# Performance work log

Hardware: AMD Instinct MI355X
Metric: run time of the kernel (lower is better)

## Reference

```python
import jax, jax.numpy as jnp
import numpy as np

B, C, F, T = 4, 64, 128, 128
K = 8        # kernel_size
H = 32       # lstm hidden size
L = 4        # lstm layers
EPS = 1e-5


def setup_inputs() -> dict:
    key = jax.random.key(0)
    ks = jax.random.split(key, 12)
    f = lambda k, s: jax.random.normal(k, s, dtype=jnp.float32) * 0.1
    return dict(
        x=jax.random.normal(ks[0], (B, C, F, T), dtype=jnp.float32),
        gamma=jnp.ones((C,), jnp.float32),
        beta=jnp.zeros((C,), jnp.float32),
        # layer 0 (input size C*K), stacked over 2 directions
        w_ih0=f(ks[1], (2, 4 * H, C * K)),
        w_hh0=f(ks[2], (2, 4 * H, H)),
        b_ih0=f(ks[3], (2, 4 * H)),
        b_hh0=f(ks[4], (2, 4 * H)),
        # layers 1..L-1 (input size 2*H), stacked [L-1, 2dirs, ...]
        w_ih=f(ks[5], (L - 1, 2, 4 * H, 2 * H)),
        w_hh=f(ks[6], (L - 1, 2, 4 * H, H)),
        b_ih=f(ks[7], (L - 1, 2, 4 * H)),
        b_hh=f(ks[8], (L - 1, 2, 4 * H)),
        # ConvTranspose1d weight, torch layout [in=2H, out=C, K]
        wct=f(ks[9], (2 * H, C, K)),
        bct=f(ks[10], (C,)),
    )


def _lstm_dir(gx, whh, reverse):
    # gx: [S, N, 4H] precomputed input projections (+ both biases)
    Hh = whh.shape[1]
    N = gx.shape[1]

    def step(carry, g):
        h, c = carry
        g = g + h @ whh.T
        i, fg, gg, o = jnp.split(g, 4, axis=-1)  # torch gate order i,f,g,o
        c = jax.nn.sigmoid(fg) * c + jax.nn.sigmoid(i) * jnp.tanh(gg)
        h = jax.nn.sigmoid(o) * jnp.tanh(c)
        return (h, c), h

    init = (jnp.zeros((N, Hh), gx.dtype), jnp.zeros((N, Hh), gx.dtype))
    _, hs = jax.lax.scan(step, init, gx, reverse=reverse)
    return hs  # [S, N, H], time-aligned with input


def _bilstm(xs, wih, whh, bih, bhh):
    outs = []
    for d, rev in ((0, False), (1, True)):
        gx = jnp.einsum('sni,gi->sng', xs, wih[d]) + bih[d] + bhh[d]
        outs.append(_lstm_dir(gx, whh[d], rev))
    return jnp.concatenate(outs, axis=-1)  # [S, N, 2H]


def reference(x, gamma, beta, w_ih0, w_hh0, b_ih0, b_hh0,
              w_ih, w_hh, b_ih, b_hh, wct, bct):
    x = jnp.swapaxes(x, -1, -2)  # [B, C, T, F]
    res = x
    Bb, Cc, Tt, Ff = x.shape
    # InstanceNorm2d (affine, biased variance over (T,F))
    mu = jnp.mean(x, axis=(2, 3), keepdims=True)
    var = jnp.var(x, axis=(2, 3), keepdims=True)
    xn = (x - mu) * jax.lax.rsqrt(var + EPS)
    xn = xn * gamma[None, :, None, None] + beta[None, :, None, None]
    # [B,F,C,T] -> [B*F, C, T]
    xf = jnp.transpose(xn, (0, 3, 1, 2)).reshape(Bb * Ff, Cc, Tt)
    # unfold(dim=2, size=K, step=1): [BF, C, T', K]
    Tp = Tt - K + 1
    idx = jnp.arange(Tp)[:, None] + jnp.arange(K)[None, :]
    seq = jnp.transpose(xf[:, :, idx], (2, 0, 1, 3)).reshape(Tp, Bb * Ff, Cc * K)
    # 4-layer bidirectional LSTM
    h = _bilstm(seq, w_ih0, w_hh0, b_ih0, b_hh0)
    for l in range(w_ih.shape[0]):
        h = _bilstm(h, w_ih[l], w_hh[l], b_ih[l], b_hh[l])
    # [S, BF, 2H] -> [BF, 2H, S]
    h = jnp.transpose(h, (1, 2, 0))
    # ConvTranspose1d stride=1, pad=0: out length = S + K - 1 = T
    y = jax.lax.conv_transpose(
        h, wct, strides=(1,), padding='VALID',
        dimension_numbers=('NCH', 'IOH', 'NCH'), transpose_kernel=True)
    y = y + bct[None, :, None]
    y = y.reshape(Bb, Ff, Cc, Tt)
    y = jnp.transpose(y, (0, 2, 3, 1)) + res  # [B, C, T, F]
    return jnp.swapaxes(y, -1, -2)  # back to [B, C, F, T]
```

## Files before the change

kernel.cpp:

```cpp
#include <hip/hip_runtime.h>

#define B_ 4
#define C_ 64
#define F_ 128
#define T_ 128
#define K_ 8
#define H_ 32
#define S_ 121
#define N_ 512
#define G_ 128
#define CK_ 512

typedef __attribute__((ext_vector_type(8))) short short8;
typedef __attribute__((ext_vector_type(4))) float f32x4;
typedef __attribute__((ext_vector_type(2))) float f32x2;
typedef __attribute__((ext_vector_type(2))) unsigned int ui2;
union FragU { uint4 u; short8 s; };

__device__ __forceinline__ unsigned int pk2(float a, float b){
  unsigned int ua = __float_as_uint(a); ua += 0x7fffu + ((ua>>16)&1u);
  unsigned int ub = __float_as_uint(b); ub += 0x7fffu + ((ub>>16)&1u);
  return (ua>>16) | (ub & 0xffff0000u);
}
__device__ __forceinline__ unsigned short bfu(float a){
  unsigned int ua = __float_as_uint(a); ua += 0x7fffu + ((ua>>16)&1u);
  return (unsigned short)(ua>>16);
}

__device__ __forceinline__ int gslot(int g){ return ((g & 63) << 1) | (g >> 6); }

__global__ __launch_bounds__(256) void k_norm(const float* __restrict__ x,
    const float* __restrict__ gamma, const float* __restrict__ beta,
    float* __restrict__ scale, float* __restrict__ shift){
  int bc = blockIdx.x;
  const float* p = x + (size_t)bc * (F_*T_);
  float s = 0.f, q = 0.f;
  for (int i = threadIdx.x; i < F_*T_; i += 256){ float v = p[i]; s += v; q += v*v; }
  #pragma unroll
  for (int o = 32; o; o >>= 1){ s += __shfl_down(s, o); q += __shfl_down(q, o); }
  __shared__ float ss[4], qq[4];
  int w = threadIdx.x >> 6;
  if ((threadIdx.x & 63) == 0){ ss[w] = s; qq[w] = q; }
  __syncthreads();
  if (threadIdx.x == 0){
    s = ss[0]+ss[1]+ss[2]+ss[3]; q = qq[0]+qq[1]+qq[2]+qq[3];
    float mu  = s / (float)(F_*T_);
    float var = q / (float)(F_*T_) - mu*mu;
    if (var < 0.f) var = 0.f;
    int c = bc & (C_-1);
    float sc = gamma[c] * rsqrtf(var + 1e-5f);
    scale[bc] = sc;
    shift[bc] = beta[c] - mu * sc;
  }
}

__global__ __launch_bounds__(256) void k_wcvt(const float* __restrict__ a,
    unsigned short* __restrict__ o, int nel){
  int i = blockIdx.x*256 + threadIdx.x;
  if (i < nel) o[i] = bfu(a[i]);
}
__global__ __launch_bounds__(256) void k_wrev(const float* __restrict__ a,
    unsigned short* __restrict__ o, int nel){
  int i = blockIdx.x*256 + threadIdx.x;
  if (i < nel){ int j = (i & ~7) | (7 - (i & 7)); o[i] = bfu(a[j]); }
}

__global__ __launch_bounds__(256) void k_gx0(const float* __restrict__ x,
    const float* __restrict__ scale, const float* __restrict__ shift,
    const unsigned short* __restrict__ wb0, const float* __restrict__ bi,
    const float* __restrict__ bh, unsigned short* __restrict__ gx){
  __shared__ unsigned int xsp[C_][80];
  int n = blockIdx.x >> 1, half = blockIdx.x & 1;
  int b = n >> 7, f = n & 127;
  const float* xb = x + (size_t)b*C_*F_*T_ + (size_t)f*T_;
  for (int i = threadIdx.x; i < C_*18; i += 256){
    int c = i / 18, q = i - c*18;
    int t0 = half*64 + q*4;
    float sc = scale[b*C_+c], sh = shift[b*C_+c];
    const float* xr = xb + (size_t)c*F_*T_;
    float4 v = (float4){0.f,0.f,0.f,0.f};
    float e = 0.f;
    bool in4 = (t0 < T_);
    if (in4) v = *(const float4*)(xr + t0);
    if (t0 + 4 < T_) e = xr[t0 + 4];
    float u0 = in4 ? v.x*sc+sh : 0.f;
    float u1 = in4 ? v.y*sc+sh : 0.f;
    float u2 = in4 ? v.z*sc+sh : 0.f;
    float u3 = in4 ? v.w*sc+sh : 0.f;
    float u4 = (t0+4 < T_) ? e*sc+sh : 0.f;
    unsigned int* xc = &xsp[c][q*4];
    xc[0] = pk2(u0,u1); xc[1] = pk2(u1,u2); xc[2] = pk2(u2,u3); xc[3] = pk2(u3,u4);
  }
  __syncthreads();
  int lane = threadIdx.x & 63, wv = threadIdx.x >> 6;
  int ln = lane & 15, quad = lane >> 4;
  int g256[4]; f32x4 acc[4][4];
  #pragma unroll
  for (int gi = 0; gi < 4; ++gi){
    g256[gi] = (wv*4 + gi)*16 + ln;
    float bv = bi[g256[gi]] + bh[g256[gi]];
    #pragma unroll
    for (int stl = 0; stl < 4; ++stl) acc[stl][gi] = (f32x4){bv, bv, bv, bv};
  }
  FragU bcur[4], bnxt[4];
  #pragma unroll
  for (int gi = 0; gi < 4; ++gi)
    bcur[gi].u = *(const uint4*)(wb0 + (size_t)g256[gi]*CK_ + quad*8);
  for (int kb = 0; kb < 16; ++kb){
    if (kb < 15){
      #pragma unroll
      for (int gi = 0; gi < 4; ++gi)
        bnxt[gi].u = *(const uint4*)(wb0 + (size_t)g256[gi]*CK_ + (kb+1)*32 + quad*8);
    }
    #pragma unroll
    for (int stl = 0; stl < 4; ++stl){
      FragU a;
      const unsigned int* rp = &xsp[kb*4 + quad][stl*16 + ln];
      a.u.x = rp[0]; a.u.y = rp[2]; a.u.z = rp[4]; a.u.w = rp[6];
      #pragma unroll
      for (int gi = 0; gi < 4; ++gi)
        acc[stl][gi] = __builtin_amdgcn_mfma_f32_16x16x32_bf16(a.s, bcur[gi].s, acc[stl][gi], 0, 0, 0);
    }
    #pragma unroll
    for (int gi = 0; gi < 4; ++gi) bcur[gi] = bnxt[gi];
  }
  #pragma unroll
  for (int stl = 0; stl < 4; ++stl)
    #pragma unroll
    for (int gi = 0; gi < 4; ++gi){
      int d = g256[gi] >> 7, g = g256[gi] & 127;
      #pragma unroll
      for (int r = 0; r < 4; ++r){
        int s = (half*4 + stl)*16 + quad*4 + r;
        if (s < S_)
          gx[((size_t)(d*N_ + n)*S_ + s)*G_ + gslot(g)] = bfu(acc[stl][gi][r]);
      }
    }
}

__global__ __launch_bounds__(128)
__attribute__((amdgpu_waves_per_eu(1, 1)))
void k_mega(const unsigned short* __restrict__ gx,
    const float* __restrict__ whh0,
    const unsigned short* __restrict__ wlb,
    const float* __restrict__ bih, const float* __restrict__ bhh,
    const float* __restrict__ whh,
    unsigned short* __restrict__ hout){
  __shared__ unsigned int rawA[64][68];
  __shared__ unsigned int rawB[64][68];
  __shared__ unsigned int glds[2][32][66];
  __shared__ unsigned int hsp[32][136];

  int n = blockIdx.x;
  int tid = threadIdx.x;
  int lane = tid & 63, d = tid >> 6;
  int j = lane & 31, hi = lane >> 5;
  int ln = lane & 15, quad = lane >> 4;

  f32x2 w1[16], w2[16];
  float hv = 0.f, c = 0.f;
  unsigned int hgd[4];
  auto rl = [&](int k)->float{
    return __uint_as_float(__builtin_amdgcn_readlane(__float_as_uint(hv), k));
  };
  auto step = [&](unsigned int cur, int u){
    float gg1 = __uint_as_float(cur << 16);
    float gg2 = __uint_as_float(cur & 0xffff0000u);
    f32x2 A1 = {gg1, 0.f}, B1 = {0.f, 0.f};
    f32x2 A2 = {gg2, 0.f}, B2 = {0.f, 0.f};
    #pragma unroll
    for (int m = 0; m < 16; m += 2){
      f32x2 h0; h0.x = rl(2*m);   h0.y = rl(2*m+1);
      f32x2 h1; h1.x = rl(2*m+2); h1.y = rl(2*m+3);
      A1 += h0*w1[m];   A2 += h0*w2[m];
      B1 += h1*w1[m+1]; B2 += h1*w2[m+1];
    }
    float acc1 = (A1.x + B1.x) + (A1.y + B1.y);
    float acc2 = (A2.x + B2.x) + (A2.y + B2.y);
    float a1 = 1.f/(1.f + __expf(-acc1));
    float x2 = hi ? acc2 : 2.f*acc2;
    float tt = 1.f/(1.f + __expf(-x2));
    float a2 = hi ? tt : 2.f*tt - 1.f;
    ui2 p1 = __builtin_amdgcn_permlane32_swap(__float_as_uint(a1), __float_as_uint(a1), false, false);
    ui2 p2 = __builtin_amdgcn_permlane32_swap(__float_as_uint(a2), __float_as_uint(a2), false, false);
    float i_ = __uint_as_float(p1.x);
    float f_ = __uint_as_float(p1.y);
    float g_ = __uint_as_float(p2.x);
    float o_ = __uint_as_float(p2.y);
    c = f_*c + i_*g_;
    float tc = 1.f/(1.f + __expf(-2.f*c));
    hv = o_*(2.f*tc - 1.f);
    unsigned int hb = (unsigned int)bfu(hv);
    if ((u & 1) == 0) hgd[u >> 1] = hb;
    else              hgd[u >> 1] |= hb << 16;
  };
  auto loadw = [&](const float* wr1, const float* wr2){
    #pragma unroll
    for (int q = 0; q < 8; ++q){
      float4 aa = *(const float4*)(wr1 + q*4);
      float4 bb = *(const float4*)(wr2 + q*4);
      w1[q*2+0] = (f32x2){aa.x, aa.y}; w1[q*2+1] = (f32x2){aa.z, aa.w};
      w2[q*2+0] = (f32x2){bb.x, bb.y}; w2[q*2+1] = (f32x2){bb.z, bb.w};
    }
    #pragma unroll
    for (int k = 0; k < 16; ++k){
      asm volatile("" : "+v"(w1[k]));
      asm volatile("" : "+v"(w2[k]));
    }
  };

  {
    loadw(whh0 + (size_t)(d*G_ + lane)*H_, whh0 + (size_t)(d*G_ + lane + 64)*H_);
    const unsigned int* gxu = (const unsigned int*)gx;
    ptrdiff_t stride = d ? -64 : 64;
    const unsigned int* p0 = gxu + ((size_t)(d*N_ + n)*S_ + (d ? (S_-1) : 0))*64 + lane;
    unsigned short* hrow = (unsigned short*)&rawA[d*32 + j][0];
    unsigned int bufA[8], bufB[8];
    #pragma unroll
    for (int u = 0; u < 8; ++u) bufA[u] = p0[stride*u];
    for (int gg = 0; gg < 7; ++gg){
      int g0 = gg*2;
      #pragma unroll
      for (int u = 0; u < 8; ++u) bufB[u] = p0[stride*(8*(g0+1) + u)];
      #pragma unroll
      for (int u = 0; u < 8; ++u) step(bufA[u], u);
      if (!hi) *(uint4*)(hrow + 8*g0) = (uint4){hgd[0], hgd[1], hgd[2], hgd[3]};
      #pragma unroll
      for (int u = 0; u < 8; ++u) bufA[u] = p0[stride*(8*(g0+2) + u)];
      #pragma unroll
      for (int u = 0; u < 8; ++u) step(bufB[u], u);
      if (!hi) *(uint4*)(hrow + 8*(g0+1)) = (uint4){hgd[0], hgd[1], hgd[2], hgd[3]};
    }
    bufB[0] = p0[stride*120];
    #pragma unroll
    for (int u = 0; u < 8; ++u) step(bufA[u], u);
    if (!hi) *(uint4*)(hrow + 112) = (uint4){hgd[0], hgd[1], hgd[2], hgd[3]};
    step(bufB[0], 0);
    if (!hi) hrow[120] = (unsigned short)(hgd[0] & 0xffffu);
  }
  __syncthreads();

  unsigned int (*rin)[68]  = rawA;
  unsigned int (*rout)[68] = rawB;
  for (int l = 0; l < 3; ++l){
    const unsigned short* rawu = (const unsigned short*)&rin[0][0];
    for (int i = tid; i < 32*128; i += 128){
      int srow = i >> 5, ip = i & 31;
      unsigned int v = 0;
      if (srow <= 120){
        int st = (ip < 16) ? srow : (120 - srow);
        v = (unsigned int)rawu[(2*ip)*136 + st] | ((unsigned int)rawu[(2*ip+1)*136 + st] << 16);
      }
      hsp[ip][srow] = v;
    }
    __syncthreads();

    const unsigned short* wp = wlb + (size_t)((l*2 + d)*G_)*64;
    float bias[8];
    const float* bip = bih + (size_t)(l*2 + d)*G_;
    const float* bhp = bhh + (size_t)(l*2 + d)*G_;
    #pragma unroll
    for (int gt = 0; gt < 8; ++gt) bias[gt] = bip[gt*16 + ln] + bhp[gt*16 + ln];
    loadw(whh + (size_t)((l*2 + d)*G_ + lane)*H_,
          whh + (size_t)((l*2 + d)*G_ + lane + 64)*H_);

    FragU bfrc[8][2];
    #pragma unroll
    for (int gt = 0; gt < 8; ++gt){
      bfrc[gt][0].u = *(const uint4*)(wp + (size_t)(gt*16 + ln)*64 + quad*8);
      bfrc[gt][1].u = *(const uint4*)(wp + (size_t)(gt*16 + ln)*64 + 32 + quad*8);
    }

    unsigned short* hrow = (unsigned short*)&rout[d*32 + j][0];
    const unsigned int* gr = &glds[d][0][lane];
    hv = 0.f; c = 0.f;

    for (int ch = 0; ch < 4; ++ch){
      int c0 = d ? (89 - 32*ch) : (32*ch);
      FragU af[2][2];
      #pragma unroll
      for (int stl = 0; stl < 2; ++stl){
        int srow = c0 + stl*16 + ln; if (srow < 0) srow = 0;
        #pragma unroll
        for (int kb = 0; kb < 2; ++kb){
          int ipb = kb*16 + quad*4;
          af[stl][kb].u.x = hsp[ipb+0][srow];
          af[stl][kb].u.y = hsp[ipb+1][srow];
          af[stl][kb].u.z = hsp[ipb+2][srow];
          af[stl][kb].u.w = hsp[ipb+3][srow];
        }
      }
      #pragma unroll
      for (int stl = 0; stl < 2; ++stl)
        #pragma unroll
        for (int gt2 = 0; gt2 < 4; ++gt2){
          f32x4 alo = (f32x4){bias[gt2],   bias[gt2],   bias[gt2],   bias[gt2]};
          f32x4 ahi = (f32x4){bias[gt2+4], bias[gt2+4], bias[gt2+4], bias[gt2+4]};
          alo = __builtin_amdgcn_mfma_f32_16x16x32_bf16(af[stl][0].s, bfrc[gt2  ][0].s, alo, 0, 0, 0);
          alo = __builtin_amdgcn_mfma_f32_16x16x32_bf16(af[stl][1].s, bfrc[gt2  ][1].s, alo, 0, 0, 0);
          ahi = __builtin_amdgcn_mfma_f32_16x16x32_bf16(af[stl][0].s, bfrc[gt2+4][0].s, ahi, 0, 0, 0);
          ahi = __builtin_amdgcn_mfma_f32_16x16x32_bf16(af[stl][1].s, bfrc[gt2+4][1].s, ahi, 0, 0, 0);
          #pragma unroll
          for (int r = 0; r < 4; ++r){
            int off = stl*16 + quad*4 + r;
            int ul = d ? (31 - off) : off;
            glds[d][ul][gt2*16 + ln] = pk2(alo[r], ahi[r]);
          }
        }
      asm volatile("" ::: "memory");
      int nfull = (ch < 3) ? 4 : 3;
      for (int gq = 0; gq < nfull; ++gq){
        unsigned int bv[8];
        #pragma unroll
        for (int u = 0; u < 8; ++u) bv[u] = gr[(gq*8 + u)*66];
        #pragma unroll
        for (int u = 0; u < 8; ++u) step(bv[u], u);
        if (!hi) *(uint4*)(hrow + ch*32 + gq*8) = (uint4){hgd[0], hgd[1], hgd[2], hgd[3]};
      }
      if (ch == 3){
        unsigned int bv0 = gr[24*66];
        step(bv0, 0);
        if (!hi) hrow[120] = (unsigned short)(hgd[0] & 0xffffu);
      }
      asm volatile("" ::: "memory");
    }
    __syncthreads();
    unsigned int (*t)[68] = rin; rin = rout; rout = t;
  }

  unsigned int* ho = (unsigned int*)hout + (size_t)n*64*64;
  for (int i = tid; i < 64*64; i += 128){
    int ci = i >> 6, k = i & 63;
    ho[ci*64 + k] = rin[ci][k];
  }
}

__global__ __launch_bounds__(256) void k_conv(const unsigned short* __restrict__ hin,
    const unsigned short* __restrict__ wA, const float* __restrict__ bct,
    const float* __restrict__ x, float* __restrict__ out){
  __shared__ unsigned int hrawL[64][65];
  __shared__ unsigned int hp2[64][144];
  int n = blockIdx.x, b = n >> 7, f = n & 127;
  const unsigned int* hu = (const unsigned int*)hin + (size_t)n*64*64;
  for (int i = threadIdx.x; i < 64*64; i += 256){
    int ci = i >> 6, k = i & 63;
    hrawL[ci][k] = hu[ci*64 + k];
  }
  __syncthreads();
  const unsigned short* rawu = (const unsigned short*)&hrawL[0][0];
  for (int it = threadIdx.x; it < 64*136; it += 256){
    int ci = it / 136, col = it - ci*136;
    int t0 = col - 8;
    int i0 = (ci < 32) ? t0 : (120 - t0);
    int i1 = (ci < 32) ? (t0+1) : (119 - t0);
    unsigned int lo  = (t0   >= 0 && t0   <= 120) ? rawu[ci*130 + i0] : 0u;
    unsigned int hi2 = (t0+1 >= 0 && t0+1 <= 120) ? rawu[ci*130 + i1] : 0u;
    hp2[ci][col] = lo | (hi2 << 16);
  }
  __syncthreads();
  int lane = threadIdx.x & 63, wv = threadIdx.x >> 6;
  int ln = lane & 15, quad = lane >> 4;
  const unsigned short* wp = wA + (size_t)(wv*16 + ln)*512;
  f32x4 acc[8];
  #pragma unroll
  for (int nt = 0; nt < 8; ++nt) acc[nt] = (f32x4){0.f,0.f,0.f,0.f};
  for (int kb = 0; kb < 16; ++kb){
    FragU afr; afr.u = *(const uint4*)(wp + kb*32 + quad*8);
    int ci = kb*4 + quad;
    #pragma unroll
    for (int nt = 0; nt < 8; ++nt){
      FragU bfr;
      const unsigned int* rp = &hp2[ci][nt*16 + ln + 1];
      bfr.u.x = rp[0]; bfr.u.y = rp[2]; bfr.u.z = rp[4]; bfr.u.w = rp[6];
      acc[nt] = __builtin_amdgcn_mfma_f32_16x16x32_bf16(afr.s, bfr.s, acc[nt], 0, 0, 0);
    }
  }
  float bb[4];
  #pragma unroll
  for (int r = 0; r < 4; ++r) bb[r] = bct[wv*16 + quad*4 + r];
  #pragma unroll
  for (int nt = 0; nt < 8; ++nt)
    #pragma unroll
    for (int r = 0; r < 4; ++r){
      int co = wv*16 + quad*4 + r, t = nt*16 + ln;
      size_t idx = ((size_t)(b*64 + co)*128 + f)*128 + t;
      out[idx] = acc[nt][r] + bb[r] + x[idx];
    }
}

extern "C" void kernel_launch(void* const* d_in, const int* in_sizes, int n_in,
                              void* d_out, int out_size, void* d_ws, size_t ws_size,
                              hipStream_t stream){
  const float* x     = (const float*)d_in[0];
  const float* gamma = (const float*)d_in[1];
  const float* beta  = (const float*)d_in[2];
  const float* wih0  = (const float*)d_in[3];
  const float* whh0  = (const float*)d_in[4];
  const float* bih0  = (const float*)d_in[5];
  const float* bhh0  = (const float*)d_in[6];
  const float* wih   = (const float*)d_in[7];
  const float* whh   = (const float*)d_in[8];
  const float* bih   = (const float*)d_in[9];
  const float* bhh   = (const float*)d_in[10];
  const float* wct   = (const float*)d_in[11];
  const float* bct   = (const float*)d_in[12];
  float* out = (float*)d_out;

  char* wsb = (char*)d_ws;
  float*          scale = (float*)(wsb);
  float*          shift = (float*)(wsb + 1024);
  unsigned short* gx    = (unsigned short*)(wsb + 2048);
  unsigned short* hA    = (unsigned short*)(wsb + 31721472);
  unsigned short* wb0   = (unsigned short*)(wsb + 48498688);
  unsigned short* wlb   = (unsigned short*)(wsb + 48760832);
  unsigned short* wcv   = (unsigned short*)(wsb + 48859136);

  k_norm<<<256, 256, 0, stream>>>(x, gamma, beta, scale, shift);
  k_wcvt<<<512, 256, 0, stream>>>(wih0, wb0, 2*G_*CK_);
  k_wcvt<<<192, 256, 0, stream>>>(wih,  wlb, 3*2*G_*64);
  k_wrev<<<128, 256, 0, stream>>>(wct,  wcv, 64*512);
  k_gx0 <<<1024, 256, 0, stream>>>(x, scale, shift, wb0, bih0, bhh0, gx);
  k_mega<<<512, 128, 0, stream>>>(gx, whh0, wlb, bih, bhh, whh, hA);
  k_conv<<<512, 256, 0, stream>>>(hA, wcv, bct, x, out);
}
```

Before: 339.7 us.

## Fuse layer-0 input projection GEMM into the LSTM mega kernel

Removes the separate k_gx0 kernel and its ~30MB bf16 gx intermediate. Each k_mega block now normalizes its own x slice into LDS and computes layer-0 gate pre-activations in 32-step chunks with MFMA before running the recurrence, staging them in LDS. This cuts a global write/read round-trip and one launch. In exchange the projection GEMM runs inside a 128-thread, one-wave-per-EU block serialized with the recurrence, and LDS regions are aliased.

```diff
diff --git a/kernel.cpp b/kernel.cpp
--- a/kernel.cpp
+++ b/kernel.cpp
@@ -26,8 +26,6 @@
   unsigned int ua = __float_as_uint(a); ua += 0x7fffu + ((ua>>16)&1u);
   return (unsigned short)(ua>>16);
 }
-
-__device__ __forceinline__ int gslot(int g){ return ((g & 63) << 1) | (g >> 6); }
 
 __global__ __launch_bounds__(256) void k_norm(const float* __restrict__ x,
     const float* __restrict__ gamma, const float* __restrict__ beta,
@@ -65,93 +63,25 @@
   if (i < nel){ int j = (i & ~7) | (7 - (i & 7)); o[i] = bfu(a[j]); }
 }
 
-__global__ __launch_bounds__(256) void k_gx0(const float* __restrict__ x,
-    const float* __restrict__ scale, const float* __restrict__ shift,
-    const unsigned short* __restrict__ wb0, const float* __restrict__ bi,
-    const float* __restrict__ bh, unsigned short* __restrict__ gx){
-  __shared__ unsigned int xsp[C_][80];
-  int n = blockIdx.x >> 1, half = blockIdx.x & 1;
-  int b = n >> 7, f = n & 127;
-  const float* xb = x + (size_t)b*C_*F_*T_ + (size_t)f*T_;
-  for (int i = threadIdx.x; i < C_*18; i += 256){
-    int c = i / 18, q = i - c*18;
-    int t0 = half*64 + q*4;
-    float sc = scale[b*C_+c], sh = shift[b*C_+c];
-    const float* xr = xb + (size_t)c*F_*T_;
-    float4 v = (float4){0.f,0.f,0.f,0.f};
-    float e = 0.f;
-    bool in4 = (t0 < T_);
-    if (in4) v = *(const float4*)(xr + t0);
-    if (t0 + 4 < T_) e = xr[t0 + 4];
-    float u0 = in4 ? v.x*sc+sh : 0.f;
-    float u1 = in4 ? v.y*sc+sh : 0.f;
-    float u2 = in4 ? v.z*sc+sh : 0.f;
-    float u3 = in4 ? v.w*sc+sh : 0.f;
-    float u4 = (t0+4 < T_) ? e*sc+sh : 0.f;
-    unsigned int* xc = &xsp[c][q*4];
-    xc[0] = pk2(u0,u1); xc[1] = pk2(u1,u2); xc[2] = pk2(u2,u3); xc[3] = pk2(u3,u4);
-  }
-  __syncthreads();
-  int lane = threadIdx.x & 63, wv = threadIdx.x >> 6;
-  int ln = lane & 15, quad = lane >> 4;
-  int g256[4]; f32x4 acc[4][4];
-  #pragma unroll
-  for (int gi = 0; gi < 4; ++gi){
-    g256[gi] = (wv*4 + gi)*16 + ln;
-    float bv = bi[g256[gi]] + bh[g256[gi]];
-    #pragma unroll
-    for (int stl = 0; stl < 4; ++stl) acc[stl][gi] = (f32x4){bv, bv, bv, bv};
-  }
-  FragU bcur[4], bnxt[4];
-  #pragma unroll
-  for (int gi = 0; gi < 4; ++gi)
-    bcur[gi].u = *(const uint4*)(wb0 + (size_t)g256[gi]*CK_ + quad*8);
-  for (int kb = 0; kb < 16; ++kb){
-    if (kb < 15){
-      #pragma unroll
-      for (int gi = 0; gi < 4; ++gi)
-        bnxt[gi].u = *(const uint4*)(wb0 + (size_t)g256[gi]*CK_ + (kb+1)*32 + quad*8);
-    }
-    #pragma unroll
-    for (int stl = 0; stl < 4; ++stl){
-      FragU a;
-      const unsigned int* rp = &xsp[kb*4 + quad][stl*16 + ln];
-      a.u.x = rp[0]; a.u.y = rp[2]; a.u.z = rp[4]; a.u.w = rp[6];
-      #pragma unroll
-      for (int gi = 0; gi < 4; ++gi)
-        acc[stl][gi] = __builtin_amdgcn_mfma_f32_16x16x32_bf16(a.s, bcur[gi].s, acc[stl][gi], 0, 0, 0);
-    }
-    #pragma unroll
-    for (int gi = 0; gi < 4; ++gi) bcur[gi] = bnxt[gi];
-  }
-  #pragma unroll
-  for (int stl = 0; stl < 4; ++stl)
-    #pragma unroll
-    for (int gi = 0; gi < 4; ++gi){
-      int d = g256[gi] >> 7, g = g256[gi] & 127;
-      #pragma unroll
-      for (int r = 0; r < 4; ++r){
-        int s = (half*4 + stl)*16 + quad*4 + r;
-        if (s < S_)
-          gx[((size_t)(d*N_ + n)*S_ + s)*G_ + gslot(g)] = bfu(acc[stl][gi][r]);
-      }
-    }
-}
-
 __global__ __launch_bounds__(128)
 __attribute__((amdgpu_waves_per_eu(1, 1)))
-void k_mega(const unsigned short* __restrict__ gx,
+void k_mega(const float* __restrict__ x,
+    const float* __restrict__ scale, const float* __restrict__ shift,
+    const unsigned short* __restrict__ wb0,
+    const float* __restrict__ bih0, const float* __restrict__ bhh0,
     const float* __restrict__ whh0,
     const unsigned short* __restrict__ wlb,
     const float* __restrict__ bih, const float* __restrict__ bhh,
     const float* __restrict__ whh,
     unsigned short* __restrict__ hout){
-  __shared__ unsigned int rawA[64][68];
-  __shared__ unsigned int rawB[64][68];
-  __shared__ unsigned int glds[2][32][66];
-  __shared__ unsigned int hsp[32][136];
-
-  int n = blockIdx.x;
+  __shared__ unsigned int smem[17280];
+  unsigned int (*rawA)[68]     = (unsigned int (*)[68])smem;
+  unsigned int (*glds)[32][66] = (unsigned int (*)[32][66])(smem + 4352);
+  unsigned int (*xsp)[136]     = (unsigned int (*)[136])(smem + 8576);
+  unsigned int (*rawB)[68]     = (unsigned int (*)[68])(smem + 8576);
+  unsigned int (*hsp)[136]     = (unsigned int (*)[136])(smem + 12928);
+
+  int n = blockIdx.x, b = n >> 7, f = n & 127;
   int tid = threadIdx.x;
   int lane = tid & 63, d = tid >> 6;
   int j = lane & 31, hi = lane >> 5;
@@ -160,9 +90,6 @@
   f32x2 w1[16], w2[16];
   float hv = 0.f, c = 0.f;
   unsigned int hgd[4];
-  auto rl = [&](int k)->float{
-    return __uint_as_float(__builtin_amdgcn_readlane(__float_as_uint(hv), k));
-  };
   auto step = [&](unsigned int cur, int u){
     float gg1 = __uint_as_float(cur << 16);
     float gg2 = __uint_as_float(cur & 0xffff0000u);
@@ -170,8 +97,11 @@
     f32x2 A2 = {gg2, 0.f}, B2 = {0.f, 0.f};
     #pragma unroll
     for (int m = 0; m < 16; m += 2){
-      f32x2 h0; h0.x = rl(2*m);   h0.y = rl(2*m+1);
-      f32x2 h1; h1.x = rl(2*m+2); h1.y = rl(2*m+3);
+      f32x2 h0, h1;
+      h0.x = __uint_as_float(__builtin_amdgcn_readlane(__float_as_uint(hv), 2*m));
+      h0.y = __uint_as_float(__builtin_amdgcn_readlane(__float_as_uint(hv), 2*m+1));
+      h1.x = __uint_as_float(__builtin_amdgcn_readlane(__float_as_uint(hv), 2*m+2));
+      h1.y = __uint_as_float(__builtin_amdgcn_readlane(__float_as_uint(hv), 2*m+3));
       A1 += h0*w1[m];   A2 += h0*w2[m];
       B1 += h1*w1[m+1]; B2 += h1*w2[m+1];
     }
@@ -210,33 +140,95 @@
   };
 
   {
+    const float* xr0 = x + (size_t)b*C_*F_*T_ + (size_t)f*T_;
+    for (int i = tid; i < 64*34; i += 128){
+      int cc = i / 34, q = i - cc*34;
+      int t0 = q*4;
+      float sc = scale[b*C_+cc], sh = shift[b*C_+cc];
+      const float* xr = xr0 + (size_t)cc*F_*T_;
+      float u0=0.f,u1=0.f,u2=0.f,u3=0.f,u4=0.f;
+      if (t0 < T_){
+        float4 v = *(const float4*)(xr + t0);
+        u0 = v.x*sc+sh; u1 = v.y*sc+sh; u2 = v.z*sc+sh; u3 = v.w*sc+sh;
+        if (t0 + 4 < T_) u4 = xr[t0+4]*sc+sh;
+      }
+      unsigned int* xc = &xsp[cc][q*4];
+      xc[0] = pk2(u0,u1); xc[1] = pk2(u1,u2); xc[2] = pk2(u2,u3); xc[3] = pk2(u3,u4);
+    }
+  }
+  __syncthreads();
+
+  {
     loadw(whh0 + (size_t)(d*G_ + lane)*H_, whh0 + (size_t)(d*G_ + lane + 64)*H_);
-    const unsigned int* gxu = (const unsigned int*)gx;
-    ptrdiff_t stride = d ? -64 : 64;
-    const unsigned int* p0 = gxu + ((size_t)(d*N_ + n)*S_ + (d ? (S_-1) : 0))*64 + lane;
+    float bias[8];
+    #pragma unroll
+    for (int gt = 0; gt < 8; ++gt)
+      bias[gt] = bih0[d*G_ + gt*16 + ln] + bhh0[d*G_ + gt*16 + ln];
+    const unsigned short* wpd = wb0 + (size_t)d*G_*CK_;
     unsigned short* hrow = (unsigned short*)&rawA[d*32 + j][0];
-    unsigned int bufA[8], bufB[8];
-    #pragma unroll
-    for (int u = 0; u < 8; ++u) bufA[u] = p0[stride*u];
-    for (int gg = 0; gg < 7; ++gg){
-      int g0 = gg*2;
+    const unsigned int* gr = &glds[d][0][lane];
+    hv = 0.f; c = 0.f;
+
+    for (int ch = 0; ch < 4; ++ch){
+      int c0 = d ? (89 - 32*ch) : (32*ch);
+      f32x4 acc[2][8];
       #pragma unroll
-      for (int u = 0; u < 8; ++u) bufB[u] = p0[stride*(8*(g0+1) + u)];
+      for (int stl = 0; stl < 2; ++stl)
+        #pragma unroll
+        for (int gt = 0; gt < 8; ++gt)
+          acc[stl][gt] = (f32x4){bias[gt], bias[gt], bias[gt], bias[gt]};
+      int sr0 = c0 + ln;      if (sr0 < 0) sr0 = 0;
+      int sr1 = c0 + 16 + ln;
+      FragU bcur[8], bnxt[8];
       #pragma unroll
-      for (int u = 0; u < 8; ++u) step(bufA[u], u);
-      if (!hi) *(uint4*)(hrow + 8*g0) = (uint4){hgd[0], hgd[1], hgd[2], hgd[3]};
+      for (int gt = 0; gt < 8; ++gt)
+        bcur[gt].u = *(const uint4*)(wpd + (size_t)(gt*16 + ln)*CK_ + quad*8);
+      for (int kb = 0; kb < 16; ++kb){
+        if (kb < 15){
+          #pragma unroll
+          for (int gt = 0; gt < 8; ++gt)
+            bnxt[gt].u = *(const uint4*)(wpd + (size_t)(gt*16 + ln)*CK_ + (kb+1)*32 + quad*8);
+        }
+        FragU a0, a1;
+        const unsigned int* rp = &xsp[kb*4 + quad][0];
+        a0.u.x = rp[sr0]; a0.u.y = rp[sr0+2]; a0.u.z = rp[sr0+4]; a0.u.w = rp[sr0+6];
+        a1.u.x = rp[sr1]; a1.u.y = rp[sr1+2]; a1.u.z = rp[sr1+4]; a1.u.w = rp[sr1+6];
+        #pragma unroll
+        for (int gt = 0; gt < 8; ++gt)
+          acc[0][gt] = __builtin_amdgcn_mfma_f32_16x16x32_bf16(a0.s, bcur[gt].s, acc[0][gt], 0, 0, 0);
+        #pragma unroll
+        for (int gt = 0; gt < 8; ++gt)
+          acc[1][gt] = __builtin_amdgcn_mfma_f32_16x16x32_bf16(a1.s, bcur[gt].s, acc[1][gt], 0, 0, 0);
+        #pragma unroll
+        for (int gt = 0; gt < 8; ++gt) bcur[gt] = bnxt[gt];
+      }
       #pragma unroll
-      for (int u = 0; u < 8; ++u) bufA[u] = p0[stride*(8*(g0+2) + u)];
-      #pragma unroll
-      for (int u = 0; u < 8; ++u) step(bufB[u], u);
-      if (!hi) *(uint4*)(hrow + 8*(g0+1)) = (uint4){hgd[0], hgd[1], hgd[2], hgd[3]};
-    }
-    bufB[0] = p0[stride*120];
-    #pragma unroll
-    for (int u = 0; u < 8; ++u) step(bufA[u], u);
-    if (!hi) *(uint4*)(hrow + 112) = (uint4){hgd[0], hgd[1], hgd[2], hgd[3]};
-    step(bufB[0], 0);
-    if (!hi) hrow[120] = (unsigned short)(hgd[0] & 0xffffu);
+      for (int stl = 0; stl < 2; ++stl)
+        #pragma unroll
+        for (int gt2 = 0; gt2 < 4; ++gt2)
+          #pragma unroll
+          for (int r = 0; r < 4; ++r){
+            int off = stl*16 + quad*4 + r;
+            int ul = d ? (31 - off) : off;
+            glds[d][ul][gt2*16 + ln] = pk2(acc[stl][gt2][r], acc[stl][gt2+4][r]);
+          }
+      asm volatile("" ::: "memory");
+      int nfull = (ch < 3) ? 4 : 3;
+      for (int gq = 0; gq < nfull; ++gq){
+        unsigned int bv[8];
+        #pragma unroll
+        for (int u = 0; u < 8; ++u) bv[u] = gr[(gq*8 + u)*66];
+        #pragma unroll
+        for (int u = 0; u < 8; ++u) step(bv[u], u);
+        if (!hi) *(uint4*)(hrow + ch*32 + gq*8) = (uint4){hgd[0], hgd[1], hgd[2], hgd[3]};
+      }
+      if (ch == 3){
+        unsigned int bv0 = gr[24*66];
+        step(bv0, 0);
+        if (!hi) hrow[120] = (unsigned short)(hgd[0] & 0xffffu);
+      }
+      asm volatile("" ::: "memory");
+    }
   }
   __syncthreads();
 
@@ -409,7 +401,6 @@
   char* wsb = (char*)d_ws;
   float*          scale = (float*)(wsb);
   float*          shift = (float*)(wsb + 1024);
-  unsigned short* gx    = (unsigned short*)(wsb + 2048);
   unsigned short* hA    = (unsigned short*)(wsb + 31721472);
   unsigned short* wb0   = (unsigned short*)(wsb + 48498688);
   unsigned short* wlb   = (unsigned short*)(wsb + 48760832);
@@ -419,7 +410,7 @@
   k_wcvt<<<512, 256, 0, stream>>>(wih0, wb0, 2*G_*CK_);
   k_wcvt<<<192, 256, 0, stream>>>(wih,  wlb, 3*2*G_*64);
   k_wrev<<<128, 256, 0, stream>>>(wct,  wcv, 64*512);
-  k_gx0 <<<1024, 256, 0, stream>>>(x, scale, shift, wb0, bih0, bhh0, gx);
-  k_mega<<<512, 128, 0, stream>>>(gx, whh0, wlb, bih, bhh, whh, hA);
+  k_mega<<<512, 128, 0, stream>>>(x, scale, shift, wb0, bih0, bhh0, whh0,
+                                  wlb, bih, bhh, whh, hA);
   k_conv<<<512, 256, 0, stream>>>(hA, wcv, bct, x, out);
 }
```

After: 384.1 us. +13.1%, slower.

## Fuse ConvTranspose epilogue into LSTM mega kernel, drop hidden-state round trip

Applied to the files above, without the earlier changes.

Moves the transposed-convolution-plus-residual stage into the end of the LSTM kernel, which reads the final hidden states directly from shared memory instead of writing them to global memory and relaunching. Shared memory is unified into one buffer, and the padded input tile is built in two halves that alias the raw buffers. Each of the two waves now computes 32 output channels with two MFMA accumulator sets. This removes a kernel launch and a global write/read of the hidden states, at the cost of only 128 threads doing the conv work and added register pressure in the occupancy-1 kernel.

```diff
diff --git a/kernel.cpp b/kernel.cpp
--- a/kernel.cpp
+++ b/kernel.cpp
@@ -145,13 +145,18 @@
     const unsigned short* __restrict__ wlb,
     const float* __restrict__ bih, const float* __restrict__ bhh,
     const float* __restrict__ whh,
-    unsigned short* __restrict__ hout){
-  __shared__ unsigned int rawA[64][68];
-  __shared__ unsigned int rawB[64][68];
-  __shared__ unsigned int glds[2][32][66];
-  __shared__ unsigned int hsp[32][136];
-
-  int n = blockIdx.x;
+    const unsigned short* __restrict__ wcv,
+    const float* __restrict__ bct,
+    const float* __restrict__ x,
+    float* __restrict__ out){
+  __shared__ unsigned int smem[17280];
+  unsigned int (*rawA)[68]     = (unsigned int (*)[68])smem;
+  unsigned int (*rawB)[68]     = (unsigned int (*)[68])(smem + 4352);
+  unsigned int (*glds)[32][66] = (unsigned int (*)[32][66])(smem + 8704);
+  unsigned int (*hsp)[136]     = (unsigned int (*)[136])(smem + 12928);
+  unsigned int (*hp2h)[136]    = (unsigned int (*)[136])smem;
+
+  int n = blockIdx.x, b = n >> 7, f = n & 127;
   int tid = threadIdx.x;
   int lane = tid & 63, d = tid >> 6;
   int j = lane & 31, hi = lane >> 5;
@@ -160,9 +165,6 @@
   f32x2 w1[16], w2[16];
   float hv = 0.f, c = 0.f;
   unsigned int hgd[4];
-  auto rl = [&](int k)->float{
-    return __uint_as_float(__builtin_amdgcn_readlane(__float_as_uint(hv), k));
-  };
   auto step = [&](unsigned int cur, int u){
     float gg1 = __uint_as_float(cur << 16);
     float gg2 = __uint_as_float(cur & 0xffff0000u);
@@ -170,8 +172,11 @@
     f32x2 A2 = {gg2, 0.f}, B2 = {0.f, 0.f};
     #pragma unroll
     for (int m = 0; m < 16; m += 2){
-      f32x2 h0; h0.x = rl(2*m);   h0.y = rl(2*m+1);
-      f32x2 h1; h1.x = rl(2*m+2); h1.y = rl(2*m+3);
+      f32x2 h0, h1;
+      h0.x = __uint_as_float(__builtin_amdgcn_readlane(__float_as_uint(hv), 2*m));
+      h0.y = __uint_as_float(__builtin_amdgcn_readlane(__float_as_uint(hv), 2*m+1));
+      h1.x = __uint_as_float(__builtin_amdgcn_readlane(__float_as_uint(hv), 2*m+2));
+      h1.y = __uint_as_float(__builtin_amdgcn_readlane(__float_as_uint(hv), 2*m+3));
       A1 += h0*w1[m];   A2 += h0*w2[m];
       B1 += h1*w1[m+1]; B2 += h1*w2[m+1];
     }
@@ -328,64 +333,58 @@
     unsigned int (*t)[68] = rin; rin = rout; rout = t;
   }
 
-  unsigned int* ho = (unsigned int*)hout + (size_t)n*64*64;
-  for (int i = tid; i < 64*64; i += 128){
-    int ci = i >> 6, k = i & 63;
-    ho[ci*64 + k] = rin[ci][k];
-  }
-}
-
-__global__ __launch_bounds__(256) void k_conv(const unsigned short* __restrict__ hin,
-    const unsigned short* __restrict__ wA, const float* __restrict__ bct,
-    const float* __restrict__ x, float* __restrict__ out){
-  __shared__ unsigned int hrawL[64][65];
-  __shared__ unsigned int hp2[64][144];
-  int n = blockIdx.x, b = n >> 7, f = n & 127;
-  const unsigned int* hu = (const unsigned int*)hin + (size_t)n*64*64;
-  for (int i = threadIdx.x; i < 64*64; i += 256){
-    int ci = i >> 6, k = i & 63;
-    hrawL[ci][k] = hu[ci*64 + k];
-  }
-  __syncthreads();
-  const unsigned short* rawu = (const unsigned short*)&hrawL[0][0];
-  for (int it = threadIdx.x; it < 64*136; it += 256){
-    int ci = it / 136, col = it - ci*136;
-    int t0 = col - 8;
-    int i0 = (ci < 32) ? t0 : (120 - t0);
-    int i1 = (ci < 32) ? (t0+1) : (119 - t0);
-    unsigned int lo  = (t0   >= 0 && t0   <= 120) ? rawu[ci*130 + i0] : 0u;
-    unsigned int hi2 = (t0+1 >= 0 && t0+1 <= 120) ? rawu[ci*130 + i1] : 0u;
-    hp2[ci][col] = lo | (hi2 << 16);
-  }
-  __syncthreads();
-  int lane = threadIdx.x & 63, wv = threadIdx.x >> 6;
-  int ln = lane & 15, quad = lane >> 4;
-  const unsigned short* wp = wA + (size_t)(wv*16 + ln)*512;
-  f32x4 acc[8];
-  #pragma unroll
-  for (int nt = 0; nt < 8; ++nt) acc[nt] = (f32x4){0.f,0.f,0.f,0.f};
-  for (int kb = 0; kb < 16; ++kb){
-    FragU afr; afr.u = *(const uint4*)(wp + kb*32 + quad*8);
-    int ci = kb*4 + quad;
-    #pragma unroll
-    for (int nt = 0; nt < 8; ++nt){
-      FragU bfr;
-      const unsigned int* rp = &hp2[ci][nt*16 + ln + 1];
-      bfr.u.x = rp[0]; bfr.u.y = rp[2]; bfr.u.z = rp[4]; bfr.u.w = rp[6];
-      acc[nt] = __builtin_amdgcn_mfma_f32_16x16x32_bf16(afr.s, bfr.s, acc[nt], 0, 0, 0);
-    }
-  }
-  float bb[4];
-  #pragma unroll
-  for (int r = 0; r < 4; ++r) bb[r] = bct[wv*16 + quad*4 + r];
-  #pragma unroll
-  for (int nt = 0; nt < 8; ++nt)
-    #pragma unroll
-    for (int r = 0; r < 4; ++r){
-      int co = wv*16 + quad*4 + r, t = nt*16 + ln;
-      size_t idx = ((size_t)(b*64 + co)*128 + f)*128 + t;
-      out[idx] = acc[nt][r] + bb[r] + x[idx];
-    }
+  {
+    f32x4 ac[2][8];
+    #pragma unroll
+    for (int cg = 0; cg < 2; ++cg)
+      #pragma unroll
+      for (int nt = 0; nt < 8; ++nt) ac[cg][nt] = (f32x4){0.f,0.f,0.f,0.f};
+    const unsigned short* wp0 = wcv + (size_t)(d*32 + ln)*512;
+    const unsigned short* wp1 = wcv + (size_t)(d*32 + 16 + ln)*512;
+    const unsigned short* rawu2 = (const unsigned short*)&rin[0][0];
+    for (int pass = 0; pass < 2; ++pass){
+      for (int it = tid; it < 32*136; it += 128){
+        int cil = it / 136, col = it - cil*136;
+        int ci = pass*32 + cil;
+        int t0 = col - 8;
+        int i0 = (ci < 32) ? t0 : (120 - t0);
+        int i1 = (ci < 32) ? (t0+1) : (119 - t0);
+        unsigned int lo  = (t0   >= 0 && t0   <= 120) ? rawu2[ci*136 + i0] : 0u;
+        unsigned int hi2 = (t0+1 >= 0 && t0+1 <= 120) ? rawu2[ci*136 + i1] : 0u;
+        hp2h[cil][col] = lo | (hi2 << 16);
+      }
+      __syncthreads();
+      for (int kb = pass*8; kb < pass*8 + 8; ++kb){
+        FragU a0, a1;
+        a0.u = *(const uint4*)(wp0 + kb*32 + quad*8);
+        a1.u = *(const uint4*)(wp1 + kb*32 + quad*8);
+        int cil = (kb - pass*8)*4 + quad;
+        #pragma unroll
+        for (int nt = 0; nt < 8; ++nt){
+          FragU bfr;
+          const unsigned int* rp = &hp2h[cil][nt*16 + ln + 1];
+          bfr.u.x = rp[0]; bfr.u.y = rp[2]; bfr.u.z = rp[4]; bfr.u.w = rp[6];
+          ac[0][nt] = __builtin_amdgcn_mfma_f32_16x16x32_bf16(a0.s, bfr.s, ac[0][nt], 0, 0, 0);
+          ac[1][nt] = __builtin_amdgcn_mfma_f32_16x16x32_bf16(a1.s, bfr.s, ac[1][nt], 0, 0, 0);
+        }
+      }
+      __syncthreads();
+    }
+    #pragma unroll
+    for (int cg = 0; cg < 2; ++cg){
+      float bb[4];
+      #pragma unroll
+      for (int r = 0; r < 4; ++r) bb[r] = bct[d*32 + cg*16 + quad*4 + r];
+      #pragma unroll
+      for (int nt = 0; nt < 8; ++nt)
+        #pragma unroll
+        for (int r = 0; r < 4; ++r){
+          int co = d*32 + cg*16 + quad*4 + r, t = nt*16 + ln;
+          size_t idx = ((size_t)(b*64 + co)*128 + f)*128 + t;
+          out[idx] = ac[cg][nt][r] + bb[r] + x[idx];
+        }
+    }
+  }
 }
 
 extern "C" void kernel_launch(void* const* d_in, const int* in_sizes, int n_in,
@@ -410,7 +409,6 @@
   float*          scale = (float*)(wsb);
   float*          shift = (float*)(wsb + 1024);
   unsigned short* gx    = (unsigned short*)(wsb + 2048);
-  unsigned short* hA    = (unsigned short*)(wsb + 31721472);
   unsigned short* wb0   = (unsigned short*)(wsb + 48498688);
   unsigned short* wlb   = (unsigned short*)(wsb + 48760832);
   unsigned short* wcv   = (unsigned short*)(wsb + 48859136);
@@ -420,6 +418,5 @@
   k_wcvt<<<192, 256, 0, stream>>>(wih,  wlb, 3*2*G_*64);
   k_wrev<<<128, 256, 0, stream>>>(wct,  wcv, 64*512);
   k_gx0 <<<1024, 256, 0, stream>>>(x, scale, shift, wb0, bih0, bhh0, gx);
-  k_mega<<<512, 128, 0, stream>>>(gx, whh0, wlb, bih, bhh, whh, hA);
-  k_conv<<<512, 256, 0, stream>>>(hA, wcv, bct, x, out);
-}
+  k_mega<<<512, 128, 0, stream>>>(gx, whh0, wlb, bih, bhh, whh, wcv, bct, x, out);
+}
```

Result: no change. 334.8 us (-1.4%).
